# Performance work log

Hardware: AMD Instinct MI355X
Metric: run time of the kernel (lower is better)

Reference implementation:

```python
import jax, jax.numpy as jnp
import numpy as np

B, T, H = 2, 2048, 1024
NUM_HEADS = 16
HEAD_DIM = H // NUM_HEADS
MAX_REL = 4


def setup_inputs() -> dict:
    key = jax.random.key(0)
    ks = jax.random.split(key, 12)
    s = 1.0 / np.sqrt(H)
    inp = {
        "x": jax.random.normal(ks[0], (B, T, H), dtype=jnp.float32),
        "text_mask": jax.random.randint(ks[1], (B, T), 0, 2, dtype=jnp.int32),
        "Wq": jax.random.normal(ks[2], (H, H), dtype=jnp.float32) * s,
        "bq": jnp.zeros((H,), dtype=jnp.float32),
        "Wk": jax.random.normal(ks[3], (H, H), dtype=jnp.float32) * s,
        "bk": jnp.zeros((H,), dtype=jnp.float32),
        "Wv": jax.random.normal(ks[4], (H, H), dtype=jnp.float32) * s,
        "bv": jnp.zeros((H,), dtype=jnp.float32),
        "Wo": jax.random.normal(ks[5], (H, H), dtype=jnp.float32) * s,
        "bo": jnp.zeros((H,), dtype=jnp.float32),
        "rel_bias": jax.random.normal(ks[6], (2 * MAX_REL + 1, NUM_HEADS), dtype=jnp.float32),
    }
    return inp


def reference(x, text_mask, Wq, bq, Wk, bk, Wv, bv, Wo, bo, rel_bias):
    b, t, h = x.shape
    scale = HEAD_DIM ** (-0.5)

    def proj(W, bias):
        # [b,t,h] -> [b,heads,t,head_dim]
        return (x @ W.T + bias).reshape(b, t, NUM_HEADS, HEAD_DIM).transpose(0, 2, 1, 3)

    q = proj(Wq, bq)
    k = proj(Wk, bk)
    v = proj(Wv, bv)

    scores = jnp.einsum("bhqd,bhkd->bhqk", q, k) * scale  # [b,heads,t,t]

    pos = jnp.arange(t)
    rel = jnp.clip(pos[None, :] - pos[:, None], -MAX_REL, MAX_REL) + MAX_REL  # [t,t]
    bias = rel_bias[rel]  # [t,t,heads]
    scores = scores + bias.transpose(2, 0, 1)[None]  # broadcast over batch

    key_valid = text_mask.astype(bool)  # [b,t]
    scores = jnp.where(key_valid[:, None, None, :], scores, -10000.0)

    attn = jax.nn.softmax(scores, axis=-1)
    hidden = jnp.einsum("bhqk,bhkd->bhqd", attn, v)
    hidden = hidden.transpose(0, 2, 1, 3).reshape(b, t, h)
    out = hidden @ Wo.T + bo
    return out * text_mask.astype(out.dtype)[:, :, None]
```

## Files before the change

### kernel.cpp

```cpp
#include <hip/hip_runtime.h>
#include <hip/hip_bf16.h>

#define B_ 2
#define T_ 2048
#define H_ 1024
#define NH 16
#define HD 64

typedef __attribute__((ext_vector_type(8))) short bf16x8;
typedef __attribute__((ext_vector_type(4))) short bf16x4;
typedef __attribute__((ext_vector_type(4))) float f32x4;

#define ASYNC_COPY16(gptr, lptr)                                              \
    __builtin_amdgcn_global_load_lds(                                         \
        (const __attribute__((address_space(1))) void*)(gptr),                \
        (__attribute__((address_space(3))) void*)(lptr), 16, 0, 0)

#if __has_builtin(__builtin_amdgcn_exp2f)
#define EXP2(x) __builtin_amdgcn_exp2f(x)
#else
static __device__ inline float EXP2(float x) {
    float r;
    asm volatile("v_exp_f32 %0, %1" : "=v"(r) : "v"(x));
    return r;
}
#endif

static __device__ inline unsigned short f2bf(float f) {
    union { float f; unsigned u; } v; v.f = f;
    unsigned r = v.u + 0x7fff + ((v.u >> 16) & 1);
    return (unsigned short)(r >> 16);
}

static __device__ inline unsigned pkbf(float a, float b) {
    float2 t2; t2.x = a; t2.y = b;
    __hip_bfloat162 h = __float22bfloat162_rn(t2);
    union { __hip_bfloat162 h; unsigned u; } cv; cv.h = h;
    return cv.u;
}

static __device__ inline bf16x4 mk4(unsigned lo, unsigned hi) {
    union { bf16x4 v; unsigned u[2]; } cv;
    cv.u[0] = lo; cv.u[1] = hi;
    return cv.v;
}

static __device__ inline f32x4 zero4() {
    f32x4 z = {0.f, 0.f, 0.f, 0.f};
    return z;
}

#define LOG2E 1.44269504088896f

__global__ void cvt_kernel(const float* __restrict__ x,
                           const float* __restrict__ wq,
                           const float* __restrict__ wk,
                           const float* __restrict__ wv,
                           const float* __restrict__ wo,
                           const int* __restrict__ maskp,
                           unsigned short* __restrict__ dst,
                           unsigned* __restrict__ cidx,
                           unsigned short* __restrict__ vidx,
                           unsigned short* __restrict__ maskc,
                           unsigned* __restrict__ meta) {
    if (blockIdx.x == 8192) {
        __shared__ unsigned ps[256];
        int t = threadIdx.x;
        int base = t * 16;
        int bb = base >> 11;
        unsigned mv = 0, cnt = 0;
#pragma unroll
        for (int i = 0; i < 16; i++) {
            if (maskp[base + i]) { mv |= (1u << i); cnt++; }
        }
        ps[t] = cnt;
        __syncthreads();
        for (int off = 1; off < 128; off <<= 1) {
            unsigned add = ((t & 127) >= off) ? ps[t - off] : 0;
            __syncthreads();
            ps[t] += add;
            __syncthreads();
        }
        unsigned cnt0 = ps[127], cnt1 = ps[255];
        unsigned ex = ps[t] - cnt;
        unsigned local = ex;
        unsigned g = (bb ? cnt0 : 0) + ex;
        for (int i = 0; i < 16; i++) {
            if (mv & (1u << i)) {
                cidx[g] = (unsigned)(base + i);
                vidx[bb * 2048 + local] =
                    (unsigned short)(base + i - bb * 2048);
                maskc[bb * 2048 + local] = 0x3F80;
                g++; local++;
            }
        }
        if (t == 0) { meta[0] = cnt0; meta[1] = cnt1; meta[2] = cnt0 + cnt1; }
        __syncthreads();
        unsigned C = cnt0 + cnt1;
        for (unsigned i = C + t; i < 4224; i += 256) cidx[i] = 0;
        for (unsigned i = cnt0 + t; i < 2048; i += 256) {
            vidx[i] = 0; maskc[i] = 0;
        }
        for (unsigned i = cnt1 + t; i < 2048; i += 256) {
            vidx[2048 + i] = 0; maskc[2048 + i] = 0;
        }
        return;
    }
    long long i0 = ((long long)blockIdx.x * blockDim.x + threadIdx.x) * 4;
    const float* src; long long off;
    if (i0 < 4194304LL)      { src = x;  off = i0; }
    else if (i0 < 5242880LL) { src = wq; off = i0 - 4194304LL; }
    else if (i0 < 6291456LL) { src = wk; off = i0 - 5242880LL; }
    else if (i0 < 7340032LL) { src = wv; off = i0 - 6291456LL; }
    else                     { src = wo; off = i0 - 7340032LL; }
    float4 f = *(const float4*)(src + off);
    ushort4 o;
    o.x = f2bf(f.x); o.y = f2bf(f.y); o.z = f2bf(f.z); o.w = f2bf(f.w);
    *(ushort4*)(dst + i0) = o;
}

__global__ __launch_bounds__(256) void qkv_gemm(
    const unsigned short* __restrict__ A,
    const unsigned short* __restrict__ Bm,
    const float* __restrict__ bq, const float* __restrict__ bk,
    const float* __restrict__ bv,
    const unsigned* __restrict__ cidx, const unsigned* __restrict__ meta,
    unsigned short* __restrict__ qout, unsigned short* __restrict__ kout,
    unsigned short* __restrict__ vout) {
    const int K = 1024;
    int C  = (int)meta[2];
    int c0 = (int)meta[0];
    int m0 = blockIdx.y * 128, n0 = blockIdx.x * 128;
    if (m0 >= C) return;
    __shared__ __align__(16) unsigned short As[128 * 32];
    __shared__ __align__(16) unsigned short Bs[128 * 32];
    int t = threadIdx.x;
    int w = t >> 6, lane = t & 63;
    int wm = (w >> 1) * 64, wn = (w & 1) * 64;
    int c = lane & 15, qd = lane >> 4;

    f32x4 acc[4][4];
#pragma unroll
    for (int i = 0; i < 4; i++)
#pragma unroll
        for (int j = 0; j < 4; j++) acc[i][j] = zero4();

    int srow = t >> 2, sseg = (t & 3) * 8;
    int r1 = (int)cidx[m0 + srow];
    int r2 = (int)cidx[m0 + srow + 64];
    const unsigned short* ag1 = A + (long long)r1 * K + sseg;
    const unsigned short* ag2 = A + (long long)r2 * K + sseg;
    const unsigned short* bg1 = Bm + (long long)(n0 + srow) * K + sseg;
    const unsigned short* bg2 = bg1 + 64LL * K;
    unsigned short* la1 = As + t * 8;
    unsigned short* la2 = As + (t + 256) * 8;
    unsigned short* lb1 = Bs + t * 8;
    unsigned short* lb2 = Bs + (t + 256) * 8;

    for (int kk = 0; kk < K; kk += 32) {
        __syncthreads();
        ASYNC_COPY16(ag1 + kk, la1);
        ASYNC_COPY16(ag2 + kk, la2);
        ASYNC_COPY16(bg1 + kk, lb1);
        ASYNC_COPY16(bg2 + kk, lb2);
        __syncthreads();
        bf16x8 af[4], bf[4];
#pragma unroll
        for (int i = 0; i < 4; i++) {
            af[i] = *(const bf16x8*)(As + (wm + i * 16 + c) * 32 + qd * 8);
            bf[i] = *(const bf16x8*)(Bs + (wn + i * 16 + c) * 32 + qd * 8);
        }
#pragma unroll
        for (int i = 0; i < 4; i++)
#pragma unroll
            for (int j = 0; j < 4; j++)
                acc[i][j] = __builtin_amdgcn_mfma_f32_16x16x32_bf16(
                    af[i], bf[j], acc[i][j], 0, 0, 0);
    }

    int gr[4][4];
#pragma unroll
    for (int i = 0; i < 4; i++)
#pragma unroll
        for (int r = 0; r < 4; r++) {
            int m = m0 + wm + i * 16 + qd * 4 + r;
            gr[i][r] = (m < C) ? (int)cidx[m] : -1;
        }

    const float QSCALE = 0.125f * LOG2E;
#pragma unroll
    for (int i = 0; i < 4; i++) {
        int m_base = m0 + wm + i * 16 + qd * 4;
#pragma unroll
        for (int j = 0; j < 4; j++) {
            int n = n0 + wn + j * 16 + c;
            int sel = n >> 10, within = n & 1023;
            int head = within >> 6, d = within & 63;
            if (sel == 0) {
                float ba = bq[within];
#pragma unroll
                for (int r = 0; r < 4; r++) {
                    if (gr[i][r] >= 0) {
                        int bb = gr[i][r] >> 11;
                        int loc = (m_base + r) - (bb ? c0 : 0);
                        qout[(((long long)(bb * NH + head)) * T_ + loc) * HD +
                             d] = f2bf((acc[i][j][r] + ba) * QSCALE);
                    }
                }
            } else if (sel == 1) {
                float ba = bk[within];
#pragma unroll
                for (int r = 0; r < 4; r++) {
                    if (gr[i][r] >= 0) {
                        int bb = gr[i][r] >> 11;
                        int loc = (m_base + r) - (bb ? c0 : 0);
                        kout[(((long long)(bb * NH + head)) * T_ + loc) * HD +
                             d] = f2bf(acc[i][j][r] + ba);
                    }
                }
            } else {
                float ba = bv[within];
                int g0 = gr[i][0], g3 = gr[i][3];
                int bb0 = g0 >> 11;
                int loc0 = m_base - (bb0 ? c0 : 0);
                if (g3 >= 0 && bb0 == (g3 >> 11) && ((loc0 & 3) == 0)) {
                    uint2 ov;
                    ov.x = pkbf(acc[i][j][0] + ba, acc[i][j][1] + ba);
                    ov.y = pkbf(acc[i][j][2] + ba, acc[i][j][3] + ba);
                    *(uint2*)(vout +
                              (((long long)(bb0 * NH + head)) * HD + d) * T_ +
                              loc0) = ov;
                } else {
#pragma unroll
                    for (int r = 0; r < 4; r++) {
                        if (gr[i][r] >= 0) {
                            int bb = gr[i][r] >> 11;
                            int loc = (m_base + r) - (bb ? c0 : 0);
                            vout[(((long long)(bb * NH + head)) * HD + d) *
                                     T_ +
                                 loc] = f2bf(acc[i][j][r] + ba);
                        }
                    }
                }
            }
        }
    }
}

__global__ __launch_bounds__(256) void out_gemm(
    const unsigned short* __restrict__ A,
    const unsigned short* __restrict__ Bm,
    const float* __restrict__ bo,
    const int* __restrict__ maskp,
    float* __restrict__ out) {
    const int K = 1024;
    __shared__ __align__(16) unsigned short As[128 * 32];
    __shared__ __align__(16) unsigned short Bs[64 * 32];
    int m0 = blockIdx.y * 128, n0 = blockIdx.x * 64;
    int t = threadIdx.x;
    int w = t >> 6, lane = t & 63;
    int wm = (w >> 1) * 64, wn = (w & 1) * 32;
    int c = lane & 15, qd = lane >> 4;

    f32x4 acc[4][2];
#pragma unroll
    for (int i = 0; i < 4; i++)
#pragma unroll
        for (int j = 0; j < 2; j++) acc[i][j] = zero4();

    int srow = t >> 2, sseg = (t & 3) * 8;
    const unsigned short* ag1 = A + (long long)(m0 + srow) * K + sseg;
    const unsigned short* ag2 = ag1 + 64LL * K;
    const unsigned short* bg1 = Bm + (long long)(n0 + srow) * K + sseg;
    unsigned short* la1 = As + t * 8;
    unsigned short* la2 = As + (t + 256) * 8;
    unsigned short* lb1 = Bs + t * 8;

    for (int kk = 0; kk < K; kk += 32) {
        __syncthreads();
        ASYNC_COPY16(ag1 + kk, la1);
        ASYNC_COPY16(ag2 + kk, la2);
        ASYNC_COPY16(bg1 + kk, lb1);
        __syncthreads();
        bf16x8 af[4], bf[2];
#pragma unroll
        for (int i = 0; i < 4; i++)
            af[i] = *(const bf16x8*)(As + (wm + i * 16 + c) * 32 + qd * 8);
#pragma unroll
        for (int j = 0; j < 2; j++)
            bf[j] = *(const bf16x8*)(Bs + (wn + j * 16 + c) * 32 + qd * 8);
#pragma unroll
        for (int i = 0; i < 4; i++)
#pragma unroll
            for (int j = 0; j < 2; j++)
                acc[i][j] = __builtin_amdgcn_mfma_f32_16x16x32_bf16(
                    af[i], bf[j], acc[i][j], 0, 0, 0);
    }

#pragma unroll
    for (int i = 0; i < 4; i++) {
#pragma unroll
        for (int j = 0; j < 2; j++) {
#pragma unroll
            for (int r = 0; r < 4; r++) {
                int m = m0 + wm + i * 16 + qd * 4 + r;
                int n = n0 + wn + j * 16 + c;
                float val = acc[i][j][r] + bo[n];
                val *= (maskp[m] != 0) ? 1.f : 0.f;
                out[(long long)m * 1024 + n] = val;
            }
        }
    }
}

__global__ __launch_bounds__(256, 2) void attn_kernel(
    const unsigned short* __restrict__ qg,
    const unsigned short* __restrict__ kg,
    const unsigned short* __restrict__ vTg,
    const float* __restrict__ rel_bias,
    const unsigned short* __restrict__ maskc,
    const unsigned short* __restrict__ vidxg,
    const unsigned* __restrict__ meta,
    unsigned short* __restrict__ hid) {
    int hb = blockIdx.x, qt = blockIdx.y;
    int h = hb & 15, b = hb >> 4;
    int cnt = (int)meta[b];
    if (qt * 128 >= cnt) return;
    int nkt = (cnt + 63) >> 6;
    int t = threadIdx.x, w = t >> 6, lane = t & 63;
    int c = lane & 15, qd = lane >> 4;

    __shared__ __align__(16) unsigned short lk[2][64 * 72];
    __shared__ __align__(16) unsigned short lvT[2][64 * 72];
    __shared__ __align__(16) unsigned short lmk[2][64];
    __shared__ __align__(16) unsigned short lki[2][64];
    __shared__ float lrbf[16];

    if (t < 9) lrbf[t] = rel_bias[t * 16 + h] * LOG2E;
    float rb0 = rel_bias[0 * 16 + h] * LOG2E;
    float rb8 = rel_bias[8 * 16 + h] * LOG2E;

    const unsigned short* qp =
        qg + (((long long)(b * NH + h)) * T_ + qt * 128) * HD;
    const unsigned short* kp = kg + ((long long)(b * NH + h)) * T_ * HD;
    const unsigned short* vp = vTg + ((long long)(b * NH + h)) * HD * T_;

    bf16x8 qf[2][2];
#pragma unroll
    for (int mt = 0; mt < 2; mt++)
#pragma unroll
        for (int ks = 0; ks < 2; ks++)
            qf[mt][ks] = *(const bf16x8*)(qp + (w * 32 + mt * 16 + c) * HD +
                                          ks * 32 + qd * 8);

    const int imin = qt * 128 + w * 32;
    int imin_t = (int)vidxg[b * 2048 + min(imin, cnt - 1)];
    int imax_t = (int)vidxg[b * 2048 + min(imin + 31, cnt - 1)];
    int itrue[2];
#pragma unroll
    for (int mt = 0; mt < 2; mt++)
        itrue[mt] =
            (int)vidxg[b * 2048 + min(imin + mt * 16 + c, cnt - 1)];

    f32x4 o[4][2];
    f32x4 lacc[2];
#pragma unroll
    for (int dt = 0; dt < 4; dt++)
#pragma unroll
        for (int mt = 0; mt < 2; mt++) o[dt][mt] = zero4();
    lacc[0] = zero4(); lacc[1] = zero4();

    int srow = t >> 2, sseg = (t & 3) * 16;
    const unsigned short* kst = kp + srow * HD + sseg;
    const unsigned short* vst = vp + srow * T_ + sseg;
    const unsigned short* mst = maskc + b * 2048 + t;
    const unsigned short* ist = vidxg + b * 2048 + t * 8;

    uint4 rk0 = *(const uint4*)(kst);
    uint4 rk1 = *(const uint4*)(kst + 8);
    uint4 rv0 = *(const uint4*)(vst);
    uint4 rv1 = *(const uint4*)(vst + 8);
    unsigned short rm = (t < 64) ? *mst : 0;
    uint4 rki = {0, 0, 0, 0};
    if (t < 8) rki = *(const uint4*)(ist);

    for (int kt = 0; kt < nkt; kt++) {
        unsigned short* KB = lk[kt & 1];
        unsigned short* VB = lvT[kt & 1];
        unsigned short* MK = lmk[kt & 1];
        unsigned short* KI = lki[kt & 1];
        *(uint4*)(KB + srow * 72 + sseg)     = rk0;
        *(uint4*)(KB + srow * 72 + sseg + 8) = rk1;
        *(uint4*)(VB + srow * 72 + sseg)     = rv0;
        *(uint4*)(VB + srow * 72 + sseg + 8) = rv1;
        if (t < 64) MK[t] = rm;
        if (t < 8) *(uint4*)(KI + t * 8) = rki;
        {
            int ktn = (kt < nkt - 1) ? kt + 1 : nkt - 1;
            rk0 = *(const uint4*)(kst + ktn * 64 * HD);
            rk1 = *(const uint4*)(kst + ktn * 64 * HD + 8);
            rv0 = *(const uint4*)(vst + ktn * 64);
            rv1 = *(const uint4*)(vst + ktn * 64 + 8);
            if (t < 64) rm = mst[ktn * 64];
            if (t < 8) rki = *(const uint4*)(ist + ktn * 64);
        }
        __syncthreads();

        int j0 = kt * 64;
        int jlo_t = (int)KI[0];
        int jhi_t = (int)KI[min(63, cnt - 1 - j0)];
        bool far_lo = (jhi_t <= imin_t - 4);
        bool far_hi = (jlo_t >= imax_t + 4);
        float ub = far_lo ? rb0 : rb8;
        bool nearband = !(far_lo || far_hi);

#pragma unroll
        for (int jt = 0; jt < 4; jt++) {
            bf16x8 kf0 = *(const bf16x8*)(KB + (jt * 16 + c) * 72 + qd * 8);
            bf16x8 kf1 =
                *(const bf16x8*)(KB + (jt * 16 + c) * 72 + 32 + qd * 8);
            bf16x4 vld4 = *(const bf16x4*)(MK + jt * 16 + qd * 4);
            ushort4 kiv = *(const ushort4*)(KI + jt * 16 + qd * 4);
            bf16x4 vf[4];
#pragma unroll
            for (int dt = 0; dt < 4; dt++)
                vf[dt] = *(const bf16x4*)(VB + (dt * 16 + c) * 72 + jt * 16 +
                                          qd * 4);
#pragma unroll
            for (int mt = 0; mt < 2; mt++) {
                f32x4 acc = zero4();
                acc = __builtin_amdgcn_mfma_f32_16x16x32_bf16(kf0, qf[mt][0],
                                                              acc, 0, 0, 0);
                acc = __builtin_amdgcn_mfma_f32_16x16x32_bf16(kf1, qf[mt][1],
                                                              acc, 0, 0, 0);
                float p0, p1, p2, p3;
                if (nearband) {
                    int it = itrue[mt];
                    int r0 = (int)kiv.x - it;
                    r0 = r0 < -4 ? -4 : (r0 > 4 ? 4 : r0);
                    int r1 = (int)kiv.y - it;
                    r1 = r1 < -4 ? -4 : (r1 > 4 ? 4 : r1);
                    int r2 = (int)kiv.z - it;
                    r2 = r2 < -4 ? -4 : (r2 > 4 ? 4 : r2);
                    int r3 = (int)kiv.w - it;
                    r3 = r3 < -4 ? -4 : (r3 > 4 ? 4 : r3);
                    p0 = EXP2(acc[0] + lrbf[r0 + 4]);
                    p1 = EXP2(acc[1] + lrbf[r1 + 4]);
                    p2 = EXP2(acc[2] + lrbf[r2 + 4]);
                    p3 = EXP2(acc[3] + lrbf[r3 + 4]);
                } else {
                    p0 = EXP2(acc[0] + ub);
                    p1 = EXP2(acc[1] + ub);
                    p2 = EXP2(acc[2] + ub);
                    p3 = EXP2(acc[3] + ub);
                }
                bf16x4 pfrag = mk4(pkbf(p0, p1), pkbf(p2, p3));
                lacc[mt] = __builtin_amdgcn_mfma_f32_16x16x16bf16_1k(
                    vld4, pfrag, lacc[mt], 0, 0, 0);
#pragma unroll
                for (int dt = 0; dt < 4; dt++)
                    o[dt][mt] = __builtin_amdgcn_mfma_f32_16x16x16bf16_1k(
                        vf[dt], pfrag, o[dt][mt], 0, 0, 0);
            }
        }
    }

#pragma unroll
    for (int mt = 0; mt < 2; mt++) {
        int rc = imin + mt * 16 + c;
        if (rc < cnt) {
            float invl = 1.0f / lacc[mt][0];
            long long row = (long long)b * T_ + itrue[mt];
#pragma unroll
            for (int dt = 0; dt < 4; dt++) {
                uint2 ov;
                ov.x = pkbf(o[dt][mt][0] * invl, o[dt][mt][1] * invl);
                ov.y = pkbf(o[dt][mt][2] * invl, o[dt][mt][3] * invl);
                *(uint2*)(hid + row * H_ + h * HD + dt * 16 + qd * 4) = ov;
            }
        }
    }
}

extern "C" void kernel_launch(void* const* d_in, const int* in_sizes, int n_in,
                              void* d_out, int out_size, void* d_ws,
                              size_t ws_size, hipStream_t stream) {
    const float* x    = (const float*)d_in[0];
    const int* maskp  = (const int*)d_in[1];
    const float* Wq   = (const float*)d_in[2];
    const float* bq   = (const float*)d_in[3];
    const float* Wk   = (const float*)d_in[4];
    const float* bk   = (const float*)d_in[5];
    const float* Wv   = (const float*)d_in[6];
    const float* bv   = (const float*)d_in[7];
    const float* Wo   = (const float*)d_in[8];
    const float* bo   = (const float*)d_in[9];
    const float* rb   = (const float*)d_in[10];
    float* out        = (float*)d_out;

    unsigned short* ws = (unsigned short*)d_ws;
    unsigned short* xb    = ws;
    unsigned short* wqkv  = ws + 4194304LL;
    unsigned short* wo_b  = ws + 7340032LL;
    unsigned short* qb    = ws + 8388608LL;
    unsigned short* kb    = ws + 12582912LL;
    unsigned short* vTb   = ws + 16777216LL;
    unsigned short* hid   = ws + 20971520LL;
    unsigned* meta        = (unsigned*)(ws + 25165824LL);
    unsigned* cidx        = (unsigned*)(ws + 25165856LL);
    unsigned short* vidx  = ws + 25174304LL;
    unsigned short* maskc = ws + 25178400LL;

    cvt_kernel<<<8193, 256, 0, stream>>>(x, Wq, Wk, Wv, Wo, maskp, ws, cidx,
                                         vidx, maskc, meta);
    qkv_gemm<<<dim3(24, 32), 256, 0, stream>>>(xb, wqkv, bq, bk, bv, cidx,
                                               meta, qb, kb, vTb);
    attn_kernel<<<dim3(32, 16), 256, 0, stream>>>(qb, kb, vTb, rb, maskc,
                                                  vidx, meta, hid);
    out_gemm<<<dim3(16, 32), 256, 0, stream>>>(hid, wo_b, bo, maskp, out);
}
```

Before: 191.5 us.

## Compact output GEMM to valid rows and shrink GEMM M-tiles to 64

The output projection now runs only on rows whose text mask is set. It gathers those rows via the compacted index and scatters results to their original positions, while masked rows are zeroed by extra blocks in the conversion kernel. Both GEMMs use 64-row tiles to cut tail waste on the compacted row count and to raise block count. The trade-off is less operand reuse per tile and an extra pass writing zeros to the output.

```diff
diff --git a/kernel.cpp b/kernel.cpp
--- a/kernel.cpp
+++ b/kernel.cpp
@@ -62,7 +62,17 @@
                            unsigned* __restrict__ cidx,
                            unsigned short* __restrict__ vidx,
                            unsigned short* __restrict__ maskc,
-                           unsigned* __restrict__ meta) {
+                           unsigned* __restrict__ meta,
+                           float* __restrict__ outz) {
+    if (blockIdx.x > 8192) {
+        long long idx =
+            ((long long)(blockIdx.x - 8193) * 256 + threadIdx.x) * 4;
+        if (idx < 4194304LL) {
+            float4 z = {0.f, 0.f, 0.f, 0.f};
+            *(float4*)(outz + idx) = z;
+        }
+        return;
+    }
     if (blockIdx.x == 8192) {
         __shared__ unsigned ps[256];
         int t = threadIdx.x;
@@ -130,57 +140,54 @@
     const int K = 1024;
     int C  = (int)meta[2];
     int c0 = (int)meta[0];
-    int m0 = blockIdx.y * 128, n0 = blockIdx.x * 128;
+    int m0 = blockIdx.y * 64, n0 = blockIdx.x * 128;
     if (m0 >= C) return;
-    __shared__ __align__(16) unsigned short As[128 * 32];
+    __shared__ __align__(16) unsigned short As[64 * 32];
     __shared__ __align__(16) unsigned short Bs[128 * 32];
     int t = threadIdx.x;
     int w = t >> 6, lane = t & 63;
-    int wm = (w >> 1) * 64, wn = (w & 1) * 64;
+    int wm = (w >> 1) * 32, wn = (w & 1) * 64;
     int c = lane & 15, qd = lane >> 4;
 
-    f32x4 acc[4][4];
-#pragma unroll
-    for (int i = 0; i < 4; i++)
+    f32x4 acc[2][4];
+#pragma unroll
+    for (int i = 0; i < 2; i++)
 #pragma unroll
         for (int j = 0; j < 4; j++) acc[i][j] = zero4();
 
     int srow = t >> 2, sseg = (t & 3) * 8;
     int r1 = (int)cidx[m0 + srow];
-    int r2 = (int)cidx[m0 + srow + 64];
     const unsigned short* ag1 = A + (long long)r1 * K + sseg;
-    const unsigned short* ag2 = A + (long long)r2 * K + sseg;
     const unsigned short* bg1 = Bm + (long long)(n0 + srow) * K + sseg;
     const unsigned short* bg2 = bg1 + 64LL * K;
     unsigned short* la1 = As + t * 8;
-    unsigned short* la2 = As + (t + 256) * 8;
     unsigned short* lb1 = Bs + t * 8;
     unsigned short* lb2 = Bs + (t + 256) * 8;
 
     for (int kk = 0; kk < K; kk += 32) {
         __syncthreads();
         ASYNC_COPY16(ag1 + kk, la1);
-        ASYNC_COPY16(ag2 + kk, la2);
         ASYNC_COPY16(bg1 + kk, lb1);
         ASYNC_COPY16(bg2 + kk, lb2);
         __syncthreads();
-        bf16x8 af[4], bf[4];
-#pragma unroll
-        for (int i = 0; i < 4; i++) {
+        bf16x8 af[2], bf[4];
+#pragma unroll
+        for (int i = 0; i < 2; i++)
             af[i] = *(const bf16x8*)(As + (wm + i * 16 + c) * 32 + qd * 8);
-            bf[i] = *(const bf16x8*)(Bs + (wn + i * 16 + c) * 32 + qd * 8);
-        }
-#pragma unroll
-        for (int i = 0; i < 4; i++)
+#pragma unroll
+        for (int j = 0; j < 4; j++)
+            bf[j] = *(const bf16x8*)(Bs + (wn + j * 16 + c) * 32 + qd * 8);
+#pragma unroll
+        for (int i = 0; i < 2; i++)
 #pragma unroll
             for (int j = 0; j < 4; j++)
                 acc[i][j] = __builtin_amdgcn_mfma_f32_16x16x32_bf16(
                     af[i], bf[j], acc[i][j], 0, 0, 0);
     }
 
-    int gr[4][4];
-#pragma unroll
-    for (int i = 0; i < 4; i++)
+    int gr[2][4];
+#pragma unroll
+    for (int i = 0; i < 2; i++)
 #pragma unroll
         for (int r = 0; r < 4; r++) {
             int m = m0 + wm + i * 16 + qd * 4 + r;
@@ -189,7 +196,7 @@
 
     const float QSCALE = 0.125f * LOG2E;
 #pragma unroll
-    for (int i = 0; i < 4; i++) {
+    for (int i = 0; i < 2; i++) {
         int m_base = m0 + wm + i * 16 + qd * 4;
 #pragma unroll
         for (int j = 0; j < 4; j++) {
@@ -251,46 +258,46 @@
     const unsigned short* __restrict__ A,
     const unsigned short* __restrict__ Bm,
     const float* __restrict__ bo,
-    const int* __restrict__ maskp,
+    const unsigned* __restrict__ cidx, const unsigned* __restrict__ meta,
     float* __restrict__ out) {
     const int K = 1024;
-    __shared__ __align__(16) unsigned short As[128 * 32];
+    int C = (int)meta[2];
+    int m0 = blockIdx.y * 64, n0 = blockIdx.x * 64;
+    if (m0 >= C) return;
+    __shared__ __align__(16) unsigned short As[64 * 32];
     __shared__ __align__(16) unsigned short Bs[64 * 32];
-    int m0 = blockIdx.y * 128, n0 = blockIdx.x * 64;
     int t = threadIdx.x;
     int w = t >> 6, lane = t & 63;
-    int wm = (w >> 1) * 64, wn = (w & 1) * 32;
+    int wm = (w >> 1) * 32, wn = (w & 1) * 32;
     int c = lane & 15, qd = lane >> 4;
 
-    f32x4 acc[4][2];
-#pragma unroll
-    for (int i = 0; i < 4; i++)
+    f32x4 acc[2][2];
+#pragma unroll
+    for (int i = 0; i < 2; i++)
 #pragma unroll
         for (int j = 0; j < 2; j++) acc[i][j] = zero4();
 
     int srow = t >> 2, sseg = (t & 3) * 8;
-    const unsigned short* ag1 = A + (long long)(m0 + srow) * K + sseg;
-    const unsigned short* ag2 = ag1 + 64LL * K;
+    int r1 = (int)cidx[m0 + srow];
+    const unsigned short* ag1 = A + (long long)r1 * K + sseg;
     const unsigned short* bg1 = Bm + (long long)(n0 + srow) * K + sseg;
     unsigned short* la1 = As + t * 8;
-    unsigned short* la2 = As + (t + 256) * 8;
     unsigned short* lb1 = Bs + t * 8;
 
     for (int kk = 0; kk < K; kk += 32) {
         __syncthreads();
         ASYNC_COPY16(ag1 + kk, la1);
-        ASYNC_COPY16(ag2 + kk, la2);
         ASYNC_COPY16(bg1 + kk, lb1);
         __syncthreads();
-        bf16x8 af[4], bf[2];
-#pragma unroll
-        for (int i = 0; i < 4; i++)
+        bf16x8 af[2], bf[2];
+#pragma unroll
+        for (int i = 0; i < 2; i++)
             af[i] = *(const bf16x8*)(As + (wm + i * 16 + c) * 32 + qd * 8);
 #pragma unroll
         for (int j = 0; j < 2; j++)
             bf[j] = *(const bf16x8*)(Bs + (wn + j * 16 + c) * 32 + qd * 8);
 #pragma unroll
-        for (int i = 0; i < 4; i++)
+        for (int i = 0; i < 2; i++)
 #pragma unroll
             for (int j = 0; j < 2; j++)
                 acc[i][j] = __builtin_amdgcn_mfma_f32_16x16x32_bf16(
@@ -298,16 +305,17 @@
     }
 
 #pragma unroll
-    for (int i = 0; i < 4; i++) {
-#pragma unroll
-        for (int j = 0; j < 2; j++) {
-#pragma unroll
-            for (int r = 0; r < 4; r++) {
-                int m = m0 + wm + i * 16 + qd * 4 + r;
-                int n = n0 + wn + j * 16 + c;
-                float val = acc[i][j][r] + bo[n];
-                val *= (maskp[m] != 0) ? 1.f : 0.f;
-                out[(long long)m * 1024 + n] = val;
+    for (int i = 0; i < 2; i++) {
+#pragma unroll
+        for (int r = 0; r < 4; r++) {
+            int m = m0 + wm + i * 16 + qd * 4 + r;
+            if (m < C) {
+                long long g = (long long)cidx[m];
+#pragma unroll
+                for (int j = 0; j < 2; j++) {
+                    int n = n0 + wn + j * 16 + c;
+                    out[g * 1024 + n] = acc[i][j][r] + bo[n];
+                }
             }
         }
     }
@@ -511,11 +519,12 @@
     unsigned short* vidx  = ws + 25174304LL;
     unsigned short* maskc = ws + 25178400LL;
 
-    cvt_kernel<<<8193, 256, 0, stream>>>(x, Wq, Wk, Wv, Wo, maskp, ws, cidx,
-                                         vidx, maskc, meta);
-    qkv_gemm<<<dim3(24, 32), 256, 0, stream>>>(xb, wqkv, bq, bk, bv, cidx,
+    cvt_kernel<<<12289, 256, 0, stream>>>(x, Wq, Wk, Wv, Wo, maskp, ws, cidx,
+                                          vidx, maskc, meta, out);
+    qkv_gemm<<<dim3(24, 64), 256, 0, stream>>>(xb, wqkv, bq, bk, bv, cidx,
                                                meta, qb, kb, vTb);
     attn_kernel<<<dim3(32, 16), 256, 0, stream>>>(qb, kb, vTb, rb, maskc,
                                                   vidx, meta, hid);
-    out_gemm<<<dim3(16, 32), 256, 0, stream>>>(hid, wo_b, bo, maskp, out);
-}
+    out_gemm<<<dim3(16, 64), 256, 0, stream>>>(hid, wo_b, bo, cidx, meta,
+                                               out);
+}
```

Result: faster. 181.9 us (-5.0%).
